# Performance work log

Hardware: AMD Instinct MI355X
Metric: run time of the kernel (lower is better)

The kernel has to match this reference:

```python
import jax, jax.numpy as jnp
import numpy as np

MACRO_CURVE_ORDER = 3
MAX_ACTION_LEN = 24
NUM_CURVES = 8
VOCAB = 361
NUM_LAYERS = 6
HID = 32


def setup_inputs() -> dict:
    key = jax.random.key(0)
    ks = iter(jax.random.split(key, 32))
    B, N_PART, P, CTX = 4096, 100, 64, 64

    def lin(k, din, dout):
        k1, k2 = jax.random.split(k)
        s = 1.0 / np.sqrt(din)
        return (jax.random.uniform(k1, (din, dout), jnp.float32, -s, s),
                jax.random.uniform(k2, (dout,), jnp.float32, -s, s))

    fc1_w, fc1_b = lin(next(ks), P, 256)
    fc2_w, fc2_b = lin(next(ks), 256, 256)
    fc3_w, fc3_b = lin(next(ks), CTX + 256, 512)
    fc4_w, fc4_b = lin(next(ks), 512, 256)
    fc5_w, fc5_b = lin(next(ks), 256, 128)
    fc6_w, fc6_b = lin(next(ks), 128, 32)
    fc10_w, fc10_b = lin(next(ks), HID, VOCAB)

    s = 1.0 / np.sqrt(HID)
    lstm_wih = jax.random.uniform(next(ks), (NUM_LAYERS, HID, 4 * HID), jnp.float32, -s, s)
    lstm_whh = jax.random.uniform(next(ks), (NUM_LAYERS, HID, 4 * HID), jnp.float32, -s, s)
    lstm_bih = jax.random.uniform(next(ks), (NUM_LAYERS, 4 * HID), jnp.float32, -s, s)
    lstm_bhh = jax.random.uniform(next(ks), (NUM_LAYERS, 4 * HID), jnp.float32, -s, s)

    return {
        "c": jax.random.normal(next(ks), (B, CTX), jnp.float32),
        "x": jax.random.normal(next(ks), (B, N_PART * P), jnp.float32),
        "hidden": jnp.zeros((NUM_LAYERS, B, HID), jnp.float32),
        "cell": jnp.zeros((NUM_LAYERS, B, HID), jnp.float32),
        "fc1_w": fc1_w, "fc1_b": fc1_b, "fc2_w": fc2_w, "fc2_b": fc2_b,
        "fc3_w": fc3_w, "fc3_b": fc3_b, "fc4_w": fc4_w, "fc4_b": fc4_b,
        "fc5_w": fc5_w, "fc5_b": fc5_b, "fc6_w": fc6_w, "fc6_b": fc6_b,
        "lstm_wih": lstm_wih, "lstm_whh": lstm_whh,
        "lstm_bih": lstm_bih, "lstm_bhh": lstm_bhh,
        "fc10_w": fc10_w, "fc10_b": fc10_b,
        "particle_size": P,
    }


def _lstm_stack(x, h, c, wih, whh, bih, bhh):
    """One time step through 6 stacked LSTM layers (PyTorch cell math)."""
    hs, cs = [], []
    inp = x
    for l in range(NUM_LAYERS):
        gates = inp @ wih[l] + bih[l] + h[l] @ whh[l] + bhh[l]  # (B, 4*HID)
        i, f, g, o = jnp.split(gates, 4, axis=-1)
        i, f, o = jax.nn.sigmoid(i), jax.nn.sigmoid(f), jax.nn.sigmoid(o)
        g = jnp.tanh(g)
        c_new = f * c[l] + i * g
        h_new = o * jnp.tanh(c_new)
        hs.append(h_new)
        cs.append(c_new)
        inp = h_new
    return inp, jnp.stack(hs), jnp.stack(cs)


def reference(c, x, hidden, cell, fc1_w, fc1_b, fc2_w, fc2_b, fc3_w, fc3_b,
              fc4_w, fc4_b, fc5_w, fc5_b, fc6_w, fc6_b,
              lstm_wih, lstm_whh, lstm_bih, lstm_bhh, fc10_w, fc10_b,
              particle_size):
    B = x.shape[0]
    # Belief (particle) encoder with mean pooling.
    xp = x.reshape(B, -1, particle_size)
    xp = jax.nn.relu(xp @ fc1_w + fc1_b)
    xp = jax.nn.relu(xp @ fc2_w + fc2_b)
    xp = xp.mean(axis=-2)  # (B, 256)
    z = jnp.concatenate([c, xp], axis=-1)
    z = jax.nn.relu(z @ fc3_w + fc3_b)
    z = jax.nn.relu(z @ fc4_w + fc4_b)
    z = jax.nn.relu(z @ fc5_w + fc5_b)
    z = jax.nn.relu(z @ fc6_w + fc6_b)  # (B, 32)

    def step(carry, _):
        xt, h, cst = carry
        xt, h, cst = _lstm_stack(xt, h, cst, lstm_wih, lstm_whh, lstm_bih, lstm_bhh)
        logits = xt @ fc10_w + fc10_b  # (B, VOCAB)
        idx = jax.lax.top_k(logits, NUM_CURVES)[1]  # (B, NUM_CURVES)
        return (xt, h, cst), idx

    (_, _, _), idxs = jax.lax.scan(step, (z, hidden, cell), None, length=MAX_ACTION_LEN)
    # (T, B, K) -> (B, T*K)
    preds = jnp.transpose(idxs, (1, 0, 2)).reshape(B, MAX_ACTION_LEN * NUM_CURVES)
    return preds
```

## Files before the change

### kernel.cpp

```cpp
#include <hip/hip_runtime.h>
#include <math.h>

#define BATCH 4096
#define NPART 100
#define PSZ   64

__device__ __forceinline__ void fma4(float4& d, const float s, const float4 v) {
    d.x = fmaf(s, v.x, d.x); d.y = fmaf(s, v.y, d.y);
    d.z = fmaf(s, v.z, d.z); d.w = fmaf(s, v.w, d.w);
}
__device__ __forceinline__ float4 addrelu4(const float4 a, const float4 b) {
    return make_float4(fmaxf(a.x + b.x, 0.f), fmaxf(a.y + b.y, 0.f),
                       fmaxf(a.z + b.z, 0.f), fmaxf(a.w + b.w, 0.f));
}

template<int NRR>
__device__ __forceinline__ void enc_chunk(
    const float* __restrict__ xb, const int rbase,
    const float* __restrict__ w1c, const float* __restrict__ w2c,
    float* __restrict__ h1s,
    const int rg, const int col0,
    const float4 b1a, const float4 b1b, const float4 b2a, const float4 b2b,
    float* msum)
{
    int rows[NRR];
    #pragma unroll
    for (int rr = 0; rr < NRR; ++rr)
        rows[rr] = rbase + ((NRR == 1) ? (rg & 3) : (rg + 8 * rr));

    float4 a0[NRR], a1[NRR];
    #pragma unroll
    for (int rr = 0; rr < NRR; ++rr) {
        a0[rr] = make_float4(0.f, 0.f, 0.f, 0.f);
        a1[rr] = make_float4(0.f, 0.f, 0.f, 0.f);
    }
    #pragma unroll 2
    for (int k0 = 0; k0 < 64; k0 += 4) {
        float4 bva[4], bvb[4];
        #pragma unroll
        for (int kk = 0; kk < 4; ++kk) {
            bva[kk] = *(const float4*)(w1c + (k0 + kk) * 256);
            bvb[kk] = *(const float4*)(w1c + (k0 + kk) * 256 + 4);
        }
        #pragma unroll
        for (int rr = 0; rr < NRR; ++rr) {
            const float4 a = *(const float4*)(xb + (size_t)rows[rr] * 64 + k0);
            fma4(a0[rr], a.x, bva[0]); fma4(a0[rr], a.y, bva[1]);
            fma4(a0[rr], a.z, bva[2]); fma4(a0[rr], a.w, bva[3]);
            fma4(a1[rr], a.x, bvb[0]); fma4(a1[rr], a.y, bvb[1]);
            fma4(a1[rr], a.z, bvb[2]); fma4(a1[rr], a.w, bvb[3]);
        }
    }
    #pragma unroll
    for (int rr = 0; rr < NRR; ++rr) {
        const int r = (NRR == 1) ? rg : (rg + 8 * rr);
        *(float4*)&h1s[r * 260 + col0]     = addrelu4(a0[rr], b1a);
        *(float4*)&h1s[r * 260 + col0 + 4] = addrelu4(a1[rr], b1b);
    }
    __syncthreads();

    float4 c0[NRR], c1[NRR];
    #pragma unroll
    for (int rr = 0; rr < NRR; ++rr) {
        c0[rr] = make_float4(0.f, 0.f, 0.f, 0.f);
        c1[rr] = make_float4(0.f, 0.f, 0.f, 0.f);
    }
    #pragma unroll 2
    for (int k0 = 0; k0 < 256; k0 += 4) {
        float4 bva[4], bvb[4];
        #pragma unroll
        for (int kk = 0; kk < 4; ++kk) {
            bva[kk] = *(const float4*)(w2c + (k0 + kk) * 256);
            bvb[kk] = *(const float4*)(w2c + (k0 + kk) * 256 + 4);
        }
        #pragma unroll
        for (int rr = 0; rr < NRR; ++rr) {
            const int r = (NRR == 1) ? rg : (rg + 8 * rr);
            const float4 a = *(const float4*)&h1s[r * 260 + k0];
            fma4(c0[rr], a.x, bva[0]); fma4(c0[rr], a.y, bva[1]);
            fma4(c0[rr], a.z, bva[2]); fma4(c0[rr], a.w, bva[3]);
            fma4(c1[rr], a.x, bvb[0]); fma4(c1[rr], a.y, bvb[1]);
            fma4(c1[rr], a.z, bvb[2]); fma4(c1[rr], a.w, bvb[3]);
        }
    }
    #pragma unroll
    for (int rr = 0; rr < NRR; ++rr) {
        if (NRR == 4 || rg < 4) {
            msum[0] += fmaxf(c0[rr].x + b2a.x, 0.f);
            msum[1] += fmaxf(c0[rr].y + b2a.y, 0.f);
            msum[2] += fmaxf(c0[rr].z + b2a.z, 0.f);
            msum[3] += fmaxf(c0[rr].w + b2a.w, 0.f);
            msum[4] += fmaxf(c1[rr].x + b2b.x, 0.f);
            msum[5] += fmaxf(c1[rr].y + b2b.y, 0.f);
            msum[6] += fmaxf(c1[rr].z + b2b.z, 0.f);
            msum[7] += fmaxf(c1[rr].w + b2b.w, 0.f);
        }
    }
    __syncthreads();
}

__global__ __launch_bounds__(256) void k_encoder(
    const float* __restrict__ x,
    const float* __restrict__ w1, const float* __restrict__ b1,
    const float* __restrict__ w2, const float* __restrict__ b2,
    float* __restrict__ xp)
{
    __shared__ __align__(16) float h1s[32 * 260];
    const int tid  = threadIdx.x;
    const int b    = blockIdx.x;
    const int lane = tid & 63;
    const int wv   = tid >> 6;
    const int cg   = lane & 7;
    const int rg   = lane >> 3;
    const int col0 = wv * 64 + cg * 8;

    const float* xb  = x + (size_t)b * (NPART * PSZ);
    const float* w1c = w1 + col0;
    const float* w2c = w2 + col0;
    const float4 b1a = *(const float4*)&b1[col0];
    const float4 b1b = *(const float4*)&b1[col0 + 4];
    const float4 b2a = *(const float4*)&b2[col0];
    const float4 b2b = *(const float4*)&b2[col0 + 4];

    float msum[8] = {0.f,0.f,0.f,0.f,0.f,0.f,0.f,0.f};

    enc_chunk<4>(xb,  0, w1c, w2c, h1s, rg, col0, b1a, b1b, b2a, b2b, msum);
    enc_chunk<4>(xb, 32, w1c, w2c, h1s, rg, col0, b1a, b1b, b2a, b2b, msum);
    enc_chunk<4>(xb, 64, w1c, w2c, h1s, rg, col0, b1a, b1b, b2a, b2b, msum);
    enc_chunk<1>(xb, 96, w1c, w2c, h1s, rg, col0, b1a, b1b, b2a, b2b, msum);

    #pragma unroll
    for (int q = 0; q < 8; ++q) {
        msum[q] += __shfl_xor(msum[q], 8, 64);
        msum[q] += __shfl_xor(msum[q], 16, 64);
        msum[q] += __shfl_xor(msum[q], 32, 64);
    }
    if (rg == 0) {
        float4 o0 = make_float4(msum[0] / 100.f, msum[1] / 100.f,
                                msum[2] / 100.f, msum[3] / 100.f);
        float4 o1 = make_float4(msum[4] / 100.f, msum[5] / 100.f,
                                msum[6] / 100.f, msum[7] / 100.f);
        *(float4*)&xp[(size_t)b * 256 + col0]     = o0;
        *(float4*)&xp[(size_t)b * 256 + col0 + 4] = o1;
    }
}

__global__ __launch_bounds__(256) void k_mlp(
    const float* __restrict__ cin, const float* __restrict__ xp,
    const float* __restrict__ w3, const float* __restrict__ b3,
    const float* __restrict__ w4, const float* __restrict__ b4,
    const float* __restrict__ w5, const float* __restrict__ b5,
    const float* __restrict__ w6, const float* __restrict__ b6,
    float* __restrict__ z)
{
    __shared__ float in0[8][320];
    __shared__ float h3[8][512];
    __shared__ float h4[8][256];
    __shared__ float h5[8][128];
    const int tid  = threadIdx.x;
    const int row0 = blockIdx.x * 8;

    for (int i = tid; i < 8 * 16; i += 256) {
        int r = i >> 4, q = i & 15;
        *(float4*)&in0[r][q * 4] = *(const float4*)&cin[(size_t)(row0 + r) * 64 + q * 4];
    }
    for (int i = tid; i < 8 * 64; i += 256) {
        int r = i >> 6, q = i & 63;
        *(float4*)&in0[r][64 + q * 4] = *(const float4*)&xp[(size_t)(row0 + r) * 256 + q * 4];
    }
    __syncthreads();

    {
        float a0[8], a1[8];
        #pragma unroll
        for (int r = 0; r < 8; ++r) { a0[r] = 0.f; a1[r] = 0.f; }
        const int c0 = tid, c1 = tid + 256;
        for (int kq = 0; kq < 80; ++kq) {
            const int k0 = kq * 4;
            float wa0 = w3[(k0+0)*512 + c0], wa1 = w3[(k0+1)*512 + c0];
            float wa2 = w3[(k0+2)*512 + c0], wa3 = w3[(k0+3)*512 + c0];
            float wb0 = w3[(k0+0)*512 + c1], wb1 = w3[(k0+1)*512 + c1];
            float wb2 = w3[(k0+2)*512 + c1], wb3 = w3[(k0+3)*512 + c1];
            #pragma unroll
            for (int r = 0; r < 8; ++r) {
                const float4 a = *(const float4*)&in0[r][k0];
                a0[r] = fmaf(a.x, wa0, fmaf(a.y, wa1, fmaf(a.z, wa2, fmaf(a.w, wa3, a0[r]))));
                a1[r] = fmaf(a.x, wb0, fmaf(a.y, wb1, fmaf(a.z, wb2, fmaf(a.w, wb3, a1[r]))));
            }
        }
        const float bb0 = b3[c0], bb1 = b3[c1];
        #pragma unroll
        for (int r = 0; r < 8; ++r) {
            h3[r][c0] = fmaxf(a0[r] + bb0, 0.f);
            h3[r][c1] = fmaxf(a1[r] + bb1, 0.f);
        }
    }
    __syncthreads();

    {
        float ac[8];
        #pragma unroll
        for (int r = 0; r < 8; ++r) ac[r] = 0.f;
        for (int kq = 0; kq < 128; ++kq) {
            const int k0 = kq * 4;
            float w0 = w4[(k0+0)*256 + tid], w1v = w4[(k0+1)*256 + tid];
            float w2v = w4[(k0+2)*256 + tid], w3v = w4[(k0+3)*256 + tid];
            #pragma unroll
            for (int r = 0; r < 8; ++r) {
                const float4 a = *(const float4*)&h3[r][k0];
                ac[r] = fmaf(a.x, w0, fmaf(a.y, w1v, fmaf(a.z, w2v, fmaf(a.w, w3v, ac[r]))));
            }
        }
        const float bb = b4[tid];
        #pragma unroll
        for (int r = 0; r < 8; ++r) h4[r][tid] = fmaxf(ac[r] + bb, 0.f);
    }
    __syncthreads();

    {
        const int c5 = tid & 127, half = tid >> 7;
        float ac[4];
        #pragma unroll
        for (int r = 0; r < 4; ++r) ac[r] = 0.f;
        for (int kq = 0; kq < 64; ++kq) {
            const int k0 = kq * 4;
            float w0 = w5[(k0+0)*128 + c5], w1v = w5[(k0+1)*128 + c5];
            float w2v = w5[(k0+2)*128 + c5], w3v = w5[(k0+3)*128 + c5];
            #pragma unroll
            for (int r = 0; r < 4; ++r) {
                const float4 a = *(const float4*)&h4[half * 4 + r][k0];
                ac[r] = fmaf(a.x, w0, fmaf(a.y, w1v, fmaf(a.z, w2v, fmaf(a.w, w3v, ac[r]))));
            }
        }
        const float bb = b5[c5];
        #pragma unroll
        for (int r = 0; r < 4; ++r) h5[half * 4 + r][c5] = fmaxf(ac[r] + bb, 0.f);
    }
    __syncthreads();

    {
        const int c6 = tid & 31, r = tid >> 5;
        float ac = 0.f;
        for (int kq = 0; kq < 32; ++kq) {
            const int k0 = kq * 4;
            float w0 = w6[(k0+0)*32 + c6], w1v = w6[(k0+1)*32 + c6];
            float w2v = w6[(k0+2)*32 + c6], w3v = w6[(k0+3)*32 + c6];
            const float4 a = *(const float4*)&h5[r][k0];
            ac = fmaf(a.x, w0, fmaf(a.y, w1v, fmaf(a.z, w2v, fmaf(a.w, w3v, ac))));
        }
        z[(size_t)(row0 + r) * 32 + c6] = fmaxf(ac + b6[c6], 0.f);
    }
}

__global__ __launch_bounds__(256) void k_lstm(
    const float* __restrict__ z,
    const float* __restrict__ hid0, const float* __restrict__ cel0,
    const float* __restrict__ wih, const float* __restrict__ whh,
    const float* __restrict__ bih, const float* __restrict__ bhh,
    const float* __restrict__ w10, const float* __restrict__ b10,
    int* __restrict__ out)
{
    __shared__ float xs[8][32];
    __shared__ float hs[6][8][32];
    __shared__ float cs[6][8][32];
    __shared__ float gates[8][128];
    __shared__ float logits[8][361];
    const int tid  = threadIdx.x;
    const int row0 = blockIdx.x * 8;

    for (int i = tid; i < 8 * 32; i += 256) xs[0][i] = z[(size_t)row0 * 32 + i];
    for (int i = tid; i < 6 * 8 * 32; i += 256) {
        int l = i >> 8, rj = i & 255;
        (&hs[0][0][0])[i] = hid0[(size_t)l * BATCH * 32 + (size_t)row0 * 32 + rj];
        (&cs[0][0][0])[i] = cel0[(size_t)l * BATCH * 32 + (size_t)row0 * 32 + rj];
    }
    __syncthreads();

    const int g  = tid & 127, rg = tid >> 7;
    const int jc = tid & 31,  jr = tid >> 5;
    const int wv = tid >> 6,  lane = tid & 63;

    for (int t = 0; t < 24; ++t) {
        for (int l = 0; l < 6; ++l) {
            const float* inp = (l == 0) ? ((t == 0) ? &xs[0][0] : &hs[5][0][0])
                                        : &hs[l - 1][0][0];
            const float* WI = wih + (size_t)l * 32 * 128;
            const float* WH = whh + (size_t)l * 32 * 128;
            const float bsum = bih[l * 128 + g] + bhh[l * 128 + g];
            float acc[4] = {bsum, bsum, bsum, bsum};
            #pragma unroll
            for (int k = 0; k < 32; k += 4) {
                float wi0 = WI[(k+0)*128 + g], wi1 = WI[(k+1)*128 + g];
                float wi2 = WI[(k+2)*128 + g], wi3 = WI[(k+3)*128 + g];
                float wh0 = WH[(k+0)*128 + g], wh1 = WH[(k+1)*128 + g];
                float wh2 = WH[(k+2)*128 + g], wh3 = WH[(k+3)*128 + g];
                #pragma unroll
                for (int rr = 0; rr < 4; ++rr) {
                    const int r = rg * 4 + rr;
                    const float4 ai = *(const float4*)&inp[r * 32 + k];
                    const float4 ah = *(const float4*)&hs[l][r][k];
                    acc[rr] = fmaf(ai.x, wi0, acc[rr]); acc[rr] = fmaf(ai.y, wi1, acc[rr]);
                    acc[rr] = fmaf(ai.z, wi2, acc[rr]); acc[rr] = fmaf(ai.w, wi3, acc[rr]);
                    acc[rr] = fmaf(ah.x, wh0, acc[rr]); acc[rr] = fmaf(ah.y, wh1, acc[rr]);
                    acc[rr] = fmaf(ah.z, wh2, acc[rr]); acc[rr] = fmaf(ah.w, wh3, acc[rr]);
                }
            }
            #pragma unroll
            for (int rr = 0; rr < 4; ++rr) gates[rg * 4 + rr][g] = acc[rr];
            __syncthreads();

            {
                const float gi = gates[jr][jc],      gf = gates[jr][32 + jc];
                const float gg = gates[jr][64 + jc], go = gates[jr][96 + jc];
                const float i_ = 1.f / (1.f + expf(-gi));
                const float f_ = 1.f / (1.f + expf(-gf));
                const float o_ = 1.f / (1.f + expf(-go));
                const float g_ = tanhf(gg);
                const float cn = f_ * cs[l][jr][jc] + i_ * g_;
                cs[l][jr][jc] = cn;
                hs[l][jr][jc] = o_ * tanhf(cn);
            }
            __syncthreads();
        }

        #pragma unroll
        for (int pass = 0; pass < 2; ++pass) {
            const int v = tid + pass * 256;
            if (v < 361) {
                const float bb = b10[v];
                float a8[8];
                #pragma unroll
                for (int r = 0; r < 8; ++r) a8[r] = bb;
                #pragma unroll
                for (int k = 0; k < 32; k += 4) {
                    float w0 = w10[(k+0)*361 + v], w1v = w10[(k+1)*361 + v];
                    float w2v = w10[(k+2)*361 + v], w3v = w10[(k+3)*361 + v];
                    #pragma unroll
                    for (int r = 0; r < 8; ++r) {
                        const float4 a = *(const float4*)&hs[5][r][k];
                        a8[r] = fmaf(a.x, w0, fmaf(a.y, w1v, fmaf(a.z, w2v, fmaf(a.w, w3v, a8[r]))));
                    }
                }
                #pragma unroll
                for (int r = 0; r < 8; ++r) logits[r][v] = a8[r];
            }
        }
        __syncthreads();

        for (int rr = 0; rr < 2; ++rr) {
            const int r = wv * 2 + rr;
            float val[6];
            #pragma unroll
            for (int s = 0; s < 6; ++s) {
                const int v = lane + 64 * s;
                val[s] = (v < 361) ? logits[r][v] : -3.4e38f;
            }
            unsigned msk = 0x3Fu;
            const int rowg = row0 + r;
            for (int sel = 0; sel < 8; ++sel) {
                float bv = -3.4e38f; int bi = 0x7FFFFFFF;
                #pragma unroll
                for (int s = 0; s < 6; ++s) {
                    if (msk & (1u << s)) {
                        const float v2 = val[s]; const int i2 = lane + 64 * s;
                        if (v2 > bv || (v2 == bv && i2 < bi)) { bv = v2; bi = i2; }
                    }
                }
                #pragma unroll
                for (int off = 32; off >= 1; off >>= 1) {
                    const float ov = __shfl_xor(bv, off, 64);
                    const int   oi = __shfl_xor(bi, off, 64);
                    if (ov > bv || (ov == bv && oi < bi)) { bv = ov; bi = oi; }
                }
                if ((bi & 63) == lane) msk &= ~(1u << (bi >> 6));
                if (lane == 0) out[(size_t)rowg * 192 + t * 8 + sel] = bi;
            }
        }
        __syncthreads();
    }
}

extern "C" void kernel_launch(void* const* d_in, const int* in_sizes, int n_in,
                              void* d_out, int out_size, void* d_ws, size_t ws_size,
                              hipStream_t stream) {
    const float* cin  = (const float*)d_in[0];
    const float* x    = (const float*)d_in[1];
    const float* hid0 = (const float*)d_in[2];
    const float* cel0 = (const float*)d_in[3];
    const float* w1 = (const float*)d_in[4];  const float* b1 = (const float*)d_in[5];
    const float* w2 = (const float*)d_in[6];  const float* b2 = (const float*)d_in[7];
    const float* w3 = (const float*)d_in[8];  const float* b3 = (const float*)d_in[9];
    const float* w4 = (const float*)d_in[10]; const float* b4 = (const float*)d_in[11];
    const float* w5 = (const float*)d_in[12]; const float* b5 = (const float*)d_in[13];
    const float* w6 = (const float*)d_in[14]; const float* b6 = (const float*)d_in[15];
    const float* wih = (const float*)d_in[16]; const float* whh = (const float*)d_in[17];
    const float* bih = (const float*)d_in[18]; const float* bhh = (const float*)d_in[19];
    const float* w10 = (const float*)d_in[20]; const float* b10 = (const float*)d_in[21];

    float* xp = (float*)d_ws;
    float* zz = xp + (size_t)BATCH * 256;
    int*   out = (int*)d_out;

    k_encoder<<<BATCH, 256, 0, stream>>>(x, w1, b1, w2, b2, xp);
    k_mlp<<<BATCH / 8, 256, 0, stream>>>(cin, xp, w3, b3, w4, b4, w5, b5, w6, b6, zz);
    k_lstm<<<BATCH / 8, 256, 0, stream>>>(zz, hid0, cel0, wih, whh, bih, bhh, w10, b10, out);
}
```

Measured before the change: 2.408 ms.

## Retile encoder to 4-column threads and run LSTM as one wave per two rows

The encoder now gives each thread 4 output columns and 8 rows instead of 8 columns and 4 rows, and adds an occupancy hint to launch bounds. The LSTM kernel becomes a single 64-lane wavefront per block handling 2 batch rows. Cell state stays in registers and no block-wide barriers are needed. A new prep kernel transposes the LSTM and output-projection weights and pre-sums the biases so the LSTM reads them as contiguous float4 loads. The cost is an extra launch, and each LSTM block reuses its weights over only 2 rows, so weight traffic through cache rises.

```diff
diff --git a/kernel.cpp b/kernel.cpp
--- a/kernel.cpp
+++ b/kernel.cpp
@@ -14,92 +14,59 @@
                        fmaxf(a.z + b.z, 0.f), fmaxf(a.w + b.w, 0.f));
 }
 
-template<int NRR>
+template<int NJ>
 __device__ __forceinline__ void enc_chunk(
     const float* __restrict__ xb, const int rbase,
     const float* __restrict__ w1c, const float* __restrict__ w2c,
-    float* __restrict__ h1s,
-    const int rg, const int col0,
-    const float4 b1a, const float4 b1b, const float4 b2a, const float4 b2b,
-    float* msum)
-{
-    int rows[NRR];
-    #pragma unroll
-    for (int rr = 0; rr < NRR; ++rr)
-        rows[rr] = rbase + ((NRR == 1) ? (rg & 3) : (rg + 8 * rr));
-
-    float4 a0[NRR], a1[NRR];
-    #pragma unroll
-    for (int rr = 0; rr < NRR; ++rr) {
-        a0[rr] = make_float4(0.f, 0.f, 0.f, 0.f);
-        a1[rr] = make_float4(0.f, 0.f, 0.f, 0.f);
-    }
+    float* __restrict__ h1s, const int rg, const int col0,
+    const float4 b1v, const float4 b2v, float4& msum)
+{
+    float4 acc1[NJ];
+    #pragma unroll
+    for (int j = 0; j < NJ; ++j) acc1[j] = make_float4(0.f, 0.f, 0.f, 0.f);
     #pragma unroll 2
     for (int k0 = 0; k0 < 64; k0 += 4) {
-        float4 bva[4], bvb[4];
-        #pragma unroll
-        for (int kk = 0; kk < 4; ++kk) {
-            bva[kk] = *(const float4*)(w1c + (k0 + kk) * 256);
-            bvb[kk] = *(const float4*)(w1c + (k0 + kk) * 256 + 4);
-        }
-        #pragma unroll
-        for (int rr = 0; rr < NRR; ++rr) {
-            const float4 a = *(const float4*)(xb + (size_t)rows[rr] * 64 + k0);
-            fma4(a0[rr], a.x, bva[0]); fma4(a0[rr], a.y, bva[1]);
-            fma4(a0[rr], a.z, bva[2]); fma4(a0[rr], a.w, bva[3]);
-            fma4(a1[rr], a.x, bvb[0]); fma4(a1[rr], a.y, bvb[1]);
-            fma4(a1[rr], a.z, bvb[2]); fma4(a1[rr], a.w, bvb[3]);
-        }
-    }
-    #pragma unroll
-    for (int rr = 0; rr < NRR; ++rr) {
-        const int r = (NRR == 1) ? rg : (rg + 8 * rr);
-        *(float4*)&h1s[r * 260 + col0]     = addrelu4(a0[rr], b1a);
-        *(float4*)&h1s[r * 260 + col0 + 4] = addrelu4(a1[rr], b1b);
-    }
-    __syncthreads();
-
-    float4 c0[NRR], c1[NRR];
-    #pragma unroll
-    for (int rr = 0; rr < NRR; ++rr) {
-        c0[rr] = make_float4(0.f, 0.f, 0.f, 0.f);
-        c1[rr] = make_float4(0.f, 0.f, 0.f, 0.f);
-    }
+        float4 w[4];
+        #pragma unroll
+        for (int kk = 0; kk < 4; ++kk)
+            w[kk] = *(const float4*)(w1c + (k0 + kk) * 256);
+        #pragma unroll
+        for (int j = 0; j < NJ; ++j) {
+            const float4 a = *(const float4*)(xb + (size_t)(rbase + rg + 4 * j) * 64 + k0);
+            fma4(acc1[j], a.x, w[0]); fma4(acc1[j], a.y, w[1]);
+            fma4(acc1[j], a.z, w[2]); fma4(acc1[j], a.w, w[3]);
+        }
+    }
+    #pragma unroll
+    for (int j = 0; j < NJ; ++j)
+        *(float4*)&h1s[(rg + 4 * j) * 260 + col0] = addrelu4(acc1[j], b1v);
+    __syncthreads();
+
+    float4 acc2[NJ];
+    #pragma unroll
+    for (int j = 0; j < NJ; ++j) acc2[j] = make_float4(0.f, 0.f, 0.f, 0.f);
     #pragma unroll 2
     for (int k0 = 0; k0 < 256; k0 += 4) {
-        float4 bva[4], bvb[4];
-        #pragma unroll
-        for (int kk = 0; kk < 4; ++kk) {
-            bva[kk] = *(const float4*)(w2c + (k0 + kk) * 256);
-            bvb[kk] = *(const float4*)(w2c + (k0 + kk) * 256 + 4);
-        }
-        #pragma unroll
-        for (int rr = 0; rr < NRR; ++rr) {
-            const int r = (NRR == 1) ? rg : (rg + 8 * rr);
-            const float4 a = *(const float4*)&h1s[r * 260 + k0];
-            fma4(c0[rr], a.x, bva[0]); fma4(c0[rr], a.y, bva[1]);
-            fma4(c0[rr], a.z, bva[2]); fma4(c0[rr], a.w, bva[3]);
-            fma4(c1[rr], a.x, bvb[0]); fma4(c1[rr], a.y, bvb[1]);
-            fma4(c1[rr], a.z, bvb[2]); fma4(c1[rr], a.w, bvb[3]);
-        }
-    }
-    #pragma unroll
-    for (int rr = 0; rr < NRR; ++rr) {
-        if (NRR == 4 || rg < 4) {
-            msum[0] += fmaxf(c0[rr].x + b2a.x, 0.f);
-            msum[1] += fmaxf(c0[rr].y + b2a.y, 0.f);
-            msum[2] += fmaxf(c0[rr].z + b2a.z, 0.f);
-            msum[3] += fmaxf(c0[rr].w + b2a.w, 0.f);
-            msum[4] += fmaxf(c1[rr].x + b2b.x, 0.f);
-            msum[5] += fmaxf(c1[rr].y + b2b.y, 0.f);
-            msum[6] += fmaxf(c1[rr].z + b2b.z, 0.f);
-            msum[7] += fmaxf(c1[rr].w + b2b.w, 0.f);
-        }
-    }
-    __syncthreads();
-}
-
-__global__ __launch_bounds__(256) void k_encoder(
+        float4 w[4];
+        #pragma unroll
+        for (int kk = 0; kk < 4; ++kk)
+            w[kk] = *(const float4*)(w2c + (k0 + kk) * 256);
+        #pragma unroll
+        for (int j = 0; j < NJ; ++j) {
+            const float4 a = *(const float4*)&h1s[(rg + 4 * j) * 260 + k0];
+            fma4(acc2[j], a.x, w[0]); fma4(acc2[j], a.y, w[1]);
+            fma4(acc2[j], a.z, w[2]); fma4(acc2[j], a.w, w[3]);
+        }
+    }
+    #pragma unroll
+    for (int j = 0; j < NJ; ++j) {
+        const float4 r = addrelu4(acc2[j], b2v);
+        msum.x += r.x; msum.y += r.y; msum.z += r.z; msum.w += r.w;
+    }
+    __syncthreads();
+}
+
+__global__ __launch_bounds__(256, 4) void k_encoder(
     const float* __restrict__ x,
     const float* __restrict__ w1, const float* __restrict__ b1,
     const float* __restrict__ w2, const float* __restrict__ b2,
@@ -110,38 +77,30 @@
     const int b    = blockIdx.x;
     const int lane = tid & 63;
     const int wv   = tid >> 6;
-    const int cg   = lane & 7;
-    const int rg   = lane >> 3;
-    const int col0 = wv * 64 + cg * 8;
+    const int cg   = lane & 15;
+    const int rg   = lane >> 4;
+    const int col0 = wv * 64 + cg * 4;
 
     const float* xb  = x + (size_t)b * (NPART * PSZ);
     const float* w1c = w1 + col0;
     const float* w2c = w2 + col0;
-    const float4 b1a = *(const float4*)&b1[col0];
-    const float4 b1b = *(const float4*)&b1[col0 + 4];
-    const float4 b2a = *(const float4*)&b2[col0];
-    const float4 b2b = *(const float4*)&b2[col0 + 4];
-
-    float msum[8] = {0.f,0.f,0.f,0.f,0.f,0.f,0.f,0.f};
-
-    enc_chunk<4>(xb,  0, w1c, w2c, h1s, rg, col0, b1a, b1b, b2a, b2b, msum);
-    enc_chunk<4>(xb, 32, w1c, w2c, h1s, rg, col0, b1a, b1b, b2a, b2b, msum);
-    enc_chunk<4>(xb, 64, w1c, w2c, h1s, rg, col0, b1a, b1b, b2a, b2b, msum);
-    enc_chunk<1>(xb, 96, w1c, w2c, h1s, rg, col0, b1a, b1b, b2a, b2b, msum);
-
-    #pragma unroll
-    for (int q = 0; q < 8; ++q) {
-        msum[q] += __shfl_xor(msum[q], 8, 64);
-        msum[q] += __shfl_xor(msum[q], 16, 64);
-        msum[q] += __shfl_xor(msum[q], 32, 64);
-    }
+    const float4 b1v = *(const float4*)&b1[col0];
+    const float4 b2v = *(const float4*)&b2[col0];
+
+    float4 ms = make_float4(0.f, 0.f, 0.f, 0.f);
+
+    enc_chunk<8>(xb,  0, w1c, w2c, h1s, rg, col0, b1v, b2v, ms);
+    enc_chunk<8>(xb, 32, w1c, w2c, h1s, rg, col0, b1v, b2v, ms);
+    enc_chunk<8>(xb, 64, w1c, w2c, h1s, rg, col0, b1v, b2v, ms);
+    enc_chunk<1>(xb, 96, w1c, w2c, h1s, rg, col0, b1v, b2v, ms);
+
+    ms.x += __shfl_xor(ms.x, 16, 64); ms.x += __shfl_xor(ms.x, 32, 64);
+    ms.y += __shfl_xor(ms.y, 16, 64); ms.y += __shfl_xor(ms.y, 32, 64);
+    ms.z += __shfl_xor(ms.z, 16, 64); ms.z += __shfl_xor(ms.z, 32, 64);
+    ms.w += __shfl_xor(ms.w, 16, 64); ms.w += __shfl_xor(ms.w, 32, 64);
     if (rg == 0) {
-        float4 o0 = make_float4(msum[0] / 100.f, msum[1] / 100.f,
-                                msum[2] / 100.f, msum[3] / 100.f);
-        float4 o1 = make_float4(msum[4] / 100.f, msum[5] / 100.f,
-                                msum[6] / 100.f, msum[7] / 100.f);
-        *(float4*)&xp[(size_t)b * 256 + col0]     = o0;
-        *(float4*)&xp[(size_t)b * 256 + col0 + 4] = o1;
+        float4 o = make_float4(ms.x / 100.f, ms.y / 100.f, ms.z / 100.f, ms.w / 100.f);
+        *(float4*)&xp[(size_t)b * 256 + col0] = o;
     }
 }
 
@@ -252,117 +211,120 @@
     }
 }
 
-__global__ __launch_bounds__(256) void k_lstm(
+__global__ __launch_bounds__(256) void k_prep(
+    const float* __restrict__ wih, const float* __restrict__ whh,
+    const float* __restrict__ bih, const float* __restrict__ bhh,
+    const float* __restrict__ w10,
+    float* __restrict__ wihT, float* __restrict__ whhT,
+    float* __restrict__ bsum, float* __restrict__ w10T)
+{
+    const int i = blockIdx.x * 256 + threadIdx.x;
+    if (i < 6 * 4096) {
+        const int l = i >> 12, r = i & 4095;
+        const int q = r >> 10, k4 = (r >> 7) & 7, c = (r >> 2) & 31, j = r & 3;
+        const int src = l * 4096 + (k4 * 4 + j) * 128 + q * 32 + c;
+        wihT[i] = wih[src];
+        whhT[i] = whh[src];
+    }
+    if (i < 361 * 32) {
+        const int v = i >> 5, k = i & 31;
+        w10T[i] = w10[k * 361 + v];
+    }
+    if (i < 768) bsum[i] = bih[i] + bhh[i];
+}
+
+__global__ __launch_bounds__(64, 4) void k_lstm(
     const float* __restrict__ z,
     const float* __restrict__ hid0, const float* __restrict__ cel0,
-    const float* __restrict__ wih, const float* __restrict__ whh,
-    const float* __restrict__ bih, const float* __restrict__ bhh,
-    const float* __restrict__ w10, const float* __restrict__ b10,
-    int* __restrict__ out)
-{
-    __shared__ float xs[8][32];
-    __shared__ float hs[6][8][32];
-    __shared__ float cs[6][8][32];
-    __shared__ float gates[8][128];
-    __shared__ float logits[8][361];
-    const int tid  = threadIdx.x;
-    const int row0 = blockIdx.x * 8;
-
-    for (int i = tid; i < 8 * 32; i += 256) xs[0][i] = z[(size_t)row0 * 32 + i];
-    for (int i = tid; i < 6 * 8 * 32; i += 256) {
-        int l = i >> 8, rj = i & 255;
-        (&hs[0][0][0])[i] = hid0[(size_t)l * BATCH * 32 + (size_t)row0 * 32 + rj];
-        (&cs[0][0][0])[i] = cel0[(size_t)l * BATCH * 32 + (size_t)row0 * 32 + rj];
-    }
-    __syncthreads();
-
-    const int g  = tid & 127, rg = tid >> 7;
-    const int jc = tid & 31,  jr = tid >> 5;
-    const int wv = tid >> 6,  lane = tid & 63;
+    const float* __restrict__ wihT, const float* __restrict__ whhT,
+    const float* __restrict__ bsum, const float* __restrict__ w10T,
+    const float* __restrict__ b10, int* __restrict__ out)
+{
+    __shared__ __align__(16) float cur[2][32];
+    __shared__ __align__(16) float hp[6][2][32];
+    const int lane = threadIdx.x;
+    const int c    = lane & 31;
+    const int rw   = lane >> 5;
+    const int row0 = blockIdx.x * 2;
+    const int row  = row0 + rw;
+
+    cur[rw][c] = z[(size_t)row * 32 + c];
+    float creg[6];
+    #pragma unroll
+    for (int l = 0; l < 6; ++l) {
+        hp[l][rw][c] = hid0[(size_t)l * BATCH * 32 + (size_t)row * 32 + c];
+        creg[l]      = cel0[(size_t)l * BATCH * 32 + (size_t)row * 32 + c];
+    }
 
     for (int t = 0; t < 24; ++t) {
+        #pragma unroll
         for (int l = 0; l < 6; ++l) {
-            const float* inp = (l == 0) ? ((t == 0) ? &xs[0][0] : &hs[5][0][0])
-                                        : &hs[l - 1][0][0];
-            const float* WI = wih + (size_t)l * 32 * 128;
-            const float* WH = whh + (size_t)l * 32 * 128;
-            const float bsum = bih[l * 128 + g] + bhh[l * 128 + g];
-            float acc[4] = {bsum, bsum, bsum, bsum};
-            #pragma unroll
-            for (int k = 0; k < 32; k += 4) {
-                float wi0 = WI[(k+0)*128 + g], wi1 = WI[(k+1)*128 + g];
-                float wi2 = WI[(k+2)*128 + g], wi3 = WI[(k+3)*128 + g];
-                float wh0 = WH[(k+0)*128 + g], wh1 = WH[(k+1)*128 + g];
-                float wh2 = WH[(k+2)*128 + g], wh3 = WH[(k+3)*128 + g];
+            float4 xi[8], hh[8];
+            #pragma unroll
+            for (int k4 = 0; k4 < 8; ++k4) {
+                xi[k4] = *(const float4*)&cur[rw][k4 * 4];
+                hh[k4] = *(const float4*)&hp[l][rw][k4 * 4];
+            }
+            const float* WI = wihT + l * 4096 + c * 4;
+            const float* WH = whhT + l * 4096 + c * 4;
+            float g4[4];
+            #pragma unroll
+            for (int q = 0; q < 4; ++q) {
+                float acc = bsum[l * 128 + q * 32 + c];
                 #pragma unroll
-                for (int rr = 0; rr < 4; ++rr) {
-                    const int r = rg * 4 + rr;
-                    const float4 ai = *(const float4*)&inp[r * 32 + k];
-                    const float4 ah = *(const float4*)&hs[l][r][k];
-                    acc[rr] = fmaf(ai.x, wi0, acc[rr]); acc[rr] = fmaf(ai.y, wi1, acc[rr]);
-                    acc[rr] = fmaf(ai.z, wi2, acc[rr]); acc[rr] = fmaf(ai.w, wi3, acc[rr]);
-                    acc[rr] = fmaf(ah.x, wh0, acc[rr]); acc[rr] = fmaf(ah.y, wh1, acc[rr]);
-                    acc[rr] = fmaf(ah.z, wh2, acc[rr]); acc[rr] = fmaf(ah.w, wh3, acc[rr]);
+                for (int k4 = 0; k4 < 8; ++k4) {
+                    const float4 wi = *(const float4*)(WI + q * 1024 + k4 * 128);
+                    const float4 wh = *(const float4*)(WH + q * 1024 + k4 * 128);
+                    acc = fmaf(xi[k4].x, wi.x, acc); acc = fmaf(xi[k4].y, wi.y, acc);
+                    acc = fmaf(xi[k4].z, wi.z, acc); acc = fmaf(xi[k4].w, wi.w, acc);
+                    acc = fmaf(hh[k4].x, wh.x, acc); acc = fmaf(hh[k4].y, wh.y, acc);
+                    acc = fmaf(hh[k4].z, wh.z, acc); acc = fmaf(hh[k4].w, wh.w, acc);
                 }
-            }
-            #pragma unroll
-            for (int rr = 0; rr < 4; ++rr) gates[rg * 4 + rr][g] = acc[rr];
-            __syncthreads();
-
-            {
-                const float gi = gates[jr][jc],      gf = gates[jr][32 + jc];
-                const float gg = gates[jr][64 + jc], go = gates[jr][96 + jc];
-                const float i_ = 1.f / (1.f + expf(-gi));
-                const float f_ = 1.f / (1.f + expf(-gf));
-                const float o_ = 1.f / (1.f + expf(-go));
-                const float g_ = tanhf(gg);
-                const float cn = f_ * cs[l][jr][jc] + i_ * g_;
-                cs[l][jr][jc] = cn;
-                hs[l][jr][jc] = o_ * tanhf(cn);
-            }
-            __syncthreads();
-        }
-
-        #pragma unroll
-        for (int pass = 0; pass < 2; ++pass) {
-            const int v = tid + pass * 256;
+                g4[q] = acc;
+            }
+            const float i_ = 1.f / (1.f + expf(-g4[0]));
+            const float f_ = 1.f / (1.f + expf(-g4[1]));
+            const float g_ = tanhf(g4[2]);
+            const float o_ = 1.f / (1.f + expf(-g4[3]));
+            const float cn = f_ * creg[l] + i_ * g_;
+            creg[l] = cn;
+            const float hn = o_ * tanhf(cn);
+            hp[l][rw][c] = hn;
+            cur[rw][c]   = hn;
+        }
+
+        float val[2][6];
+        #pragma unroll
+        for (int s = 0; s < 6; ++s) {
+            const int v = lane + 64 * s;
             if (v < 361) {
-                const float bb = b10[v];
-                float a8[8];
+                const float* wv = w10T + v * 32;
+                float a0 = b10[v], a1 = a0;
                 #pragma unroll
-                for (int r = 0; r < 8; ++r) a8[r] = bb;
-                #pragma unroll
-                for (int k = 0; k < 32; k += 4) {
-                    float w0 = w10[(k+0)*361 + v], w1v = w10[(k+1)*361 + v];
-                    float w2v = w10[(k+2)*361 + v], w3v = w10[(k+3)*361 + v];
-                    #pragma unroll
-                    for (int r = 0; r < 8; ++r) {
-                        const float4 a = *(const float4*)&hs[5][r][k];
-                        a8[r] = fmaf(a.x, w0, fmaf(a.y, w1v, fmaf(a.z, w2v, fmaf(a.w, w3v, a8[r]))));
-                    }
+                for (int k4 = 0; k4 < 8; ++k4) {
+                    const float4 w  = *(const float4*)(wv + k4 * 4);
+                    const float4 h0 = *(const float4*)&cur[0][k4 * 4];
+                    const float4 h1 = *(const float4*)&cur[1][k4 * 4];
+                    a0 = fmaf(h0.x, w.x, a0); a0 = fmaf(h0.y, w.y, a0);
+                    a0 = fmaf(h0.z, w.z, a0); a0 = fmaf(h0.w, w.w, a0);
+                    a1 = fmaf(h1.x, w.x, a1); a1 = fmaf(h1.y, w.y, a1);
+                    a1 = fmaf(h1.z, w.z, a1); a1 = fmaf(h1.w, w.w, a1);
                 }
-                #pragma unroll
-                for (int r = 0; r < 8; ++r) logits[r][v] = a8[r];
-            }
-        }
-        __syncthreads();
-
-        for (int rr = 0; rr < 2; ++rr) {
-            const int r = wv * 2 + rr;
-            float val[6];
-            #pragma unroll
-            for (int s = 0; s < 6; ++s) {
-                const int v = lane + 64 * s;
-                val[s] = (v < 361) ? logits[r][v] : -3.4e38f;
-            }
+                val[0][s] = a0; val[1][s] = a1;
+            } else {
+                val[0][s] = -3.4e38f; val[1][s] = -3.4e38f;
+            }
+        }
+
+        #pragma unroll
+        for (int r = 0; r < 2; ++r) {
             unsigned msk = 0x3Fu;
-            const int rowg = row0 + r;
             for (int sel = 0; sel < 8; ++sel) {
                 float bv = -3.4e38f; int bi = 0x7FFFFFFF;
                 #pragma unroll
                 for (int s = 0; s < 6; ++s) {
                     if (msk & (1u << s)) {
-                        const float v2 = val[s]; const int i2 = lane + 64 * s;
+                        const float v2 = val[r][s]; const int i2 = lane + 64 * s;
                         if (v2 > bv || (v2 == bv && i2 < bi)) { bv = v2; bi = i2; }
                     }
                 }
@@ -373,10 +335,9 @@
                     if (ov > bv || (ov == bv && oi < bi)) { bv = ov; bi = oi; }
                 }
                 if ((bi & 63) == lane) msk &= ~(1u << (bi >> 6));
-                if (lane == 0) out[(size_t)rowg * 192 + t * 8 + sel] = bi;
-            }
-        }
-        __syncthreads();
+                if (lane == 0) out[(size_t)(row0 + r) * 192 + t * 8 + sel] = bi;
+            }
+        }
     }
 }
 
@@ -397,11 +358,16 @@
     const float* bih = (const float*)d_in[18]; const float* bhh = (const float*)d_in[19];
     const float* w10 = (const float*)d_in[20]; const float* b10 = (const float*)d_in[21];
 
-    float* xp = (float*)d_ws;
-    float* zz = xp + (size_t)BATCH * 256;
-    int*   out = (int*)d_out;
-
+    float* xp   = (float*)d_ws;
+    float* zz   = xp + (size_t)BATCH * 256;
+    float* wihT = zz + (size_t)BATCH * 32;
+    float* whhT = wihT + 6 * 4096;
+    float* bsum = whhT + 6 * 4096;
+    float* w10T = bsum + 768;
+    int*   out  = (int*)d_out;
+
+    k_prep<<<96, 256, 0, stream>>>(wih, whh, bih, bhh, w10, wihT, whhT, bsum, w10T);
     k_encoder<<<BATCH, 256, 0, stream>>>(x, w1, b1, w2, b2, xp);
     k_mlp<<<BATCH / 8, 256, 0, stream>>>(cin, xp, w3, b3, w4, b4, w5, b5, w6, b6, zz);
-    k_lstm<<<BATCH / 8, 256, 0, stream>>>(zz, hid0, cel0, wih, whh, bih, bhh, w10, b10, out);
-}
+    k_lstm<<<BATCH / 2, 64, 0, stream>>>(zz, hid0, cel0, wihT, whhT, bsum, w10T, b10, out);
+}
```

Measured after the change: 7.267 ms. +201.8%, slower.
